# Performance work log

Hardware: AMD Instinct MI355X
Metric: run time of the kernel (lower is better)

## Reference

```python
import math
import jax, jax.numpy as jnp
import numpy as np

NUM_HEADS = 8
FACTOR = 5


def setup_inputs() -> dict:
    key = jax.random.key(0)
    ks = jax.random.split(key, 5)
    B, S, D = 8, 2048, 512
    s = 1.0 / math.sqrt(D)
    return {
        "x": jax.random.normal(ks[0], (B, S, D), dtype=jnp.float32),
        "wq": jax.random.normal(ks[1], (D, D), dtype=jnp.float32) * s,
        "bq": jnp.zeros((D,), jnp.float32),
        "wk": jax.random.normal(ks[2], (D, D), dtype=jnp.float32) * s,
        "bk": jnp.zeros((D,), jnp.float32),
        "wv": jax.random.normal(ks[3], (D, D), dtype=jnp.float32) * s,
        "bv": jnp.zeros((D,), jnp.float32),
        "wo": jax.random.normal(ks[4], (D, D), dtype=jnp.float32) * s,
        "bo": jnp.zeros((D,), jnp.float32),
    }


def reference(x, wq, bq, wk, bk, wv, bv, wo, bo):
    B, S, Dm = x.shape
    H = NUM_HEADS
    Dh = Dm // H
    scale = jnp.sqrt(jnp.float32(Dh))
    # u = min(factor * ceil(ln(S)), S); S is static so compute in Python
    u = min(FACTOR * int(math.ceil(math.log(S))), S)

    def split_heads(t):  # [B,S,Dm] -> [B,H,S,Dh]
        return t.reshape(B, S, H, Dh).transpose(0, 2, 1, 3)

    q = split_heads(x @ wq + bq)
    k = split_heads(x @ wk + bk)
    v = split_heads(x @ wv + bv)

    # S >= 64 -> sparse branch (static decision).
    # Full logits only to compute sparsity measure M (max - mean over keys).
    logits = jnp.einsum("bhqd,bhkd->bhqk", q, k) / scale  # [B,H,S,S]
    M = jnp.max(logits, axis=-1) - jnp.mean(logits, axis=-1)  # [B,H,S]
    _, top_idx = jax.lax.top_k(M, u)  # [B,H,u]

    # Gather top-u queries and run dense attention only for them.
    q_top = jnp.take_along_axis(q, top_idx[..., None], axis=2)  # [B,H,u,Dh]
    top_logits = jnp.einsum("bhqd,bhkd->bhqk", q_top, k) / scale  # [B,H,u,S]
    top_w = jax.nn.softmax(top_logits, axis=-1)
    top_out = jnp.einsum("bhqk,bhkd->bhqd", top_w, v)  # [B,H,u,Dh]

    # Non-selected queries get the mean of V; scatter top outputs in.
    out = jnp.broadcast_to(jnp.mean(v, axis=2, keepdims=True), v.shape)
    b_idx = jnp.arange(B)[:, None, None]
    h_idx = jnp.arange(H)[None, :, None]
    out = out.at[b_idx, h_idx, top_idx].set(top_out)  # [B,H,S,Dh]

    out = out.transpose(0, 2, 1, 3).reshape(B, S, Dm)
    return out @ wo + bo
```

## Files before the change

### kernel.cpp

```cpp
#include <hip/hip_runtime.h>
#include <hip/hip_bf16.h>
#include <math.h>

#define NB 8
#define NS 2048
#define ND 512
#define NH 8
#define DHD 64
#define NU 40
#define NBH 64
#define NM 16384

typedef __attribute__((ext_vector_type(8))) short short8;
typedef __attribute__((ext_vector_type(4))) short short4v;
typedef __attribute__((ext_vector_type(4))) float f32x4;

__device__ __forceinline__ short f2bf(float f) {
  __hip_bfloat16 h = __float2bfloat16(f);
  return *reinterpret_cast<short*>(&h);
}
__device__ __forceinline__ float bf2f(short s) {
  __hip_bfloat16 h;
  *reinterpret_cast<short*>(&h) = s;
  return __bfloat162float(h);
}

__device__ __forceinline__ void gload_lds16(const short* g, short* l) {
  __builtin_amdgcn_global_load_lds(
      (const __attribute__((address_space(1))) unsigned int*)g,
      (__attribute__((address_space(3))) unsigned int*)l, 16, 0, 0);
}

__global__ void prep(const float* __restrict__ x, const float* __restrict__ w0,
                     const float* __restrict__ w1, const float* __restrict__ w2,
                     short* __restrict__ Xs, short* __restrict__ Wts) {
  if (blockIdx.x < 8192) {
    int i = blockIdx.x * 256 + threadIdx.x;
    const float4 v = *(const float4*)(x + (size_t)i * 4);
    int row = i >> 7;
    int col = (i & 127) << 2;
    float vv[4] = {v.x, v.y, v.z, v.w};
    short4v hi, lo;
#pragma unroll
    for (int j = 0; j < 4; ++j) {
      short h = f2bf(vv[j]);
      hi[j] = h;
      lo[j] = f2bf(vv[j] - bf2f(h));
    }
    *(short4v*)(Xs + (size_t)row * 1024 + col) = hi;
    *(short4v*)(Xs + (size_t)row * 1024 + 512 + col) = lo;
  } else {
    int bw = blockIdx.x - 8192;
    int y = bw >> 8;
    int bxy = bw & 255;
    const float* W = y == 0 ? w0 : y == 1 ? w1 : w2;
    short* dst = Wts + (size_t)y * 512 * 1024;
    __shared__ float tile[32][33];
    int bx = bxy & 15, by = bxy >> 4;
    int k0 = bx * 32, n0 = by * 32;
    int r = threadIdx.x >> 3, cg = (threadIdx.x & 7) * 4;
    const float4 v = *(const float4*)(W + (size_t)(k0 + r) * 512 + n0 + cg);
    tile[r][cg] = v.x; tile[r][cg + 1] = v.y; tile[r][cg + 2] = v.z; tile[r][cg + 3] = v.w;
    __syncthreads();
#pragma unroll
    for (int j = 0; j < 4; ++j) {
      int kk = cg + j;
      float f = tile[kk][r];
      short h = f2bf(f);
      dst[(size_t)(n0 + r) * 1024 + k0 + kk] = h;
      dst[(size_t)(n0 + r) * 1024 + 512 + k0 + kk] = f2bf(f - bf2f(h));
    }
  }
}

__global__ __launch_bounds__(256, 2) void qkvgemm(
    const short* __restrict__ A, const short* __restrict__ Wts,
    const float* __restrict__ bq, const float* __restrict__ bk,
    const float* __restrict__ bv, short* __restrict__ Qs,
    short* __restrict__ Ks, short* __restrict__ Vs) {
  __shared__ short As[2][128][64];
  __shared__ short Bs[2][128][64];
  const int bid = blockIdx.x;
  const int wgid = (bid & 7) * 192 + (bid >> 3);
  const int mb = wgid / 12, y = wgid % 12;
  const int m0 = mb * 128;
  const int wsel = y >> 2;
  const int n0 = (y & 3) * 128;
  const short* Wb = Wts + (size_t)wsel * 512 * 1024;
  const float* bias = wsel == 0 ? bq : wsel == 1 ? bk : bv;
  short* dstbase = wsel == 0 ? Qs : wsel == 1 ? Ks : Vs;

  const int tid = threadIdx.x;
  const int w = tid >> 6, lane = tid & 63;
  const int wm = (w >> 1) * 64, wn = (w & 1) * 64;
  const int fr = lane & 15, fk = lane >> 4;

  f32x4 acc[4][4];
  const f32x4 zz = {0.f, 0.f, 0.f, 0.f};
#pragma unroll
  for (int i = 0; i < 4; ++i)
#pragma unroll
    for (int j = 0; j < 4; ++j) acc[i][j] = zz;

  auto stage = [&](int buf, int kt) {
#pragma unroll
    for (int p = 0; p < 4; ++p) {
      int idx = (p * 4 + w) * 64 + lane;
      int r = idx >> 3, c = idx & 7;
      int cs = c ^ (r & 7);
      int sc = (cs < 4) ? (kt + cs * 8) : (512 + kt + (cs - 4) * 8);
      short* lA = &As[buf][0][0] + (p * 4 + w) * 512;
      short* lB = &Bs[buf][0][0] + (p * 4 + w) * 512;
      gload_lds16(A + (size_t)(m0 + r) * 1024 + sc, lA);
      gload_lds16(Wb + (size_t)(n0 + r) * 1024 + sc, lB);
    }
  };

  stage(0, 0);
  __syncthreads();
  for (int kt = 0; kt < 512; kt += 32) {
    int cur = (kt >> 5) & 1;
    if (kt + 32 < 512) stage(cur ^ 1, kt + 32);
    short8 ah[4], al[4], bh[4], bl[4];
#pragma unroll
    for (int mf = 0; mf < 4; ++mf) {
      int r = wm + mf * 16 + fr;
      ah[mf] = *(const short8*)&As[cur][r][(fk ^ (r & 7)) << 3];
      al[mf] = *(const short8*)&As[cur][r][((4 + fk) ^ (r & 7)) << 3];
    }
#pragma unroll
    for (int nf = 0; nf < 4; ++nf) {
      int r = wn + nf * 16 + fr;
      bh[nf] = *(const short8*)&Bs[cur][r][(fk ^ (r & 7)) << 3];
      bl[nf] = *(const short8*)&Bs[cur][r][((4 + fk) ^ (r & 7)) << 3];
    }
#pragma unroll
    for (int mf = 0; mf < 4; ++mf)
#pragma unroll
      for (int nf = 0; nf < 4; ++nf) {
        acc[mf][nf] = __builtin_amdgcn_mfma_f32_16x16x32_bf16(bh[nf], ah[mf], acc[mf][nf], 0, 0, 0);
        acc[mf][nf] = __builtin_amdgcn_mfma_f32_16x16x32_bf16(bh[nf], al[mf], acc[mf][nf], 0, 0, 0);
        acc[mf][nf] = __builtin_amdgcn_mfma_f32_16x16x32_bf16(bl[nf], ah[mf], acc[mf][nf], 0, 0, 0);
      }
    __syncthreads();
  }

#pragma unroll
  for (int mf = 0; mf < 4; ++mf) {
    int m = m0 + wm + mf * 16 + fr;
    int b = m >> 11, s = m & 2047;
#pragma unroll
    for (int nf = 0; nf < 4; ++nf) {
      int nb = n0 + wn + nf * 16 + fk * 4;
      float4 bi4 = *(const float4*)(bias + nb);
      int h = nb >> 6, dh = nb & 63;
      short* dst = dstbase + ((size_t)((b << 3) + h) * 2048 + s) * 128;
      short4v hi, lo;
      float bb[4] = {bi4.x, bi4.y, bi4.z, bi4.w};
#pragma unroll
      for (int j = 0; j < 4; ++j) {
        float v = acc[mf][nf][j] + bb[j];
        short hs = f2bf(v);
        hi[j] = hs;
        lo[j] = f2bf(v - bf2f(hs));
      }
      *(short4v*)(dst + dh) = hi;
      *(short4v*)(dst + 64 + dh) = lo;
    }
  }
}

__global__ __launch_bounds__(256) void colmeans(const short* __restrict__ K,
                                                const short* __restrict__ V,
                                                float* __restrict__ kbarf,
                                                float* __restrict__ vbarf) {
  const int bh = blockIdx.x >> 2, part = blockIdx.x & 3;
  const int c = threadIdx.x & 15;
  const int g = threadIdx.x >> 4;
  const int s0 = part * 512 + g * 32;
  const short* Kb = K + (size_t)bh * 2048 * 128;
  const short* Vb = V + (size_t)bh * 2048 * 128;
  float sk[8], sv[8];
#pragma unroll
  for (int e = 0; e < 8; ++e) { sk[e] = 0.f; sv[e] = 0.f; }
  for (int s = s0; s < s0 + 32; ++s) {
    short8 k8 = *(const short8*)(Kb + (size_t)s * 128 + c * 8);
    short8 v8 = *(const short8*)(Vb + (size_t)s * 128 + c * 8);
#pragma unroll
    for (int e = 0; e < 8; ++e) { sk[e] += bf2f(k8[e]); sv[e] += bf2f(v8[e]); }
  }
  __shared__ float rk[16][128], rv[16][128];
#pragma unroll
  for (int e = 0; e < 8; ++e) { rk[g][c * 8 + e] = sk[e]; rv[g][c * 8 + e] = sv[e]; }
  __syncthreads();
  if (threadIdx.x < 64) {
    int d = threadIdx.x;
    float a = 0.f, b2 = 0.f;
    for (int g2 = 0; g2 < 16; ++g2) {
      a += rk[g2][d] + rk[g2][64 + d];
      b2 += rv[g2][d] + rv[g2][64 + d];
    }
    atomicAdd(kbarf + bh * 64 + d, a * (1.f / 2048.f));
    atomicAdd(vbarf + bh * 64 + d, b2 * (1.f / 2048.f));
  }
}

__global__ __launch_bounds__(256, 2) void qkmax(const short* __restrict__ Qs,
                                                const short* __restrict__ Ks,
                                                const float* __restrict__ kbarf,
                                                float* __restrict__ Mval) {
  __shared__ short Kt[2][128][128];
  __shared__ float red[4][128];
  const int bid = blockIdx.x;
  const int wgid = (bid & 7) * 128 + (bid >> 3);
  const int bh = wgid >> 4, q0 = (wgid & 15) * 128;
  const short* Qb = Qs + ((size_t)bh * 2048 + q0) * 128;
  const short* Kb = Ks + (size_t)bh * 2048 * 128;
  const int tid = threadIdx.x, w = tid >> 6, lane = tid & 63;
  const int fr = lane & 15, fk = lane >> 4;

  short8 qf[8][2][2];
#pragma unroll
  for (int mf = 0; mf < 8; ++mf) {
    int row = mf * 16 + fr;
#pragma unroll
    for (int hl = 0; hl < 2; ++hl)
#pragma unroll
      for (int k0 = 0; k0 < 2; ++k0)
        qf[mf][hl][k0] =
            *(const short8*)(Qb + (size_t)row * 128 + hl * 64 + k0 * 32 + fk * 8);
  }

  f32x4 rmax[8];
#pragma unroll
  for (int mf = 0; mf < 8; ++mf)
#pragma unroll
    for (int j = 0; j < 4; ++j) rmax[mf][j] = -1e30f;
  const f32x4 zz = {0.f, 0.f, 0.f, 0.f};

  auto stageK = [&](int buf, int t) {
#pragma unroll
    for (int p = 0; p < 8; ++p) {
      int idx = p * 256 + tid;
      int r = idx >> 4, c = idx & 15;
      int cs = c ^ (r & 15);
      short* lb = &Kt[buf][0][0] + (size_t)(p * 256 + w * 64) * 8;
      gload_lds16(Kb + (size_t)(t * 128 + r) * 128 + cs * 8, lb);
    }
  };

  stageK(0, 0);
  __syncthreads();
  for (int t = 0; t < 16; ++t) {
    const int cur = t & 1;
    if (t < 15) stageK(cur ^ 1, t + 1);
#pragma unroll
    for (int nf = 0; nf < 2; ++nf) {
      int r = w * 32 + nf * 16 + fr;
      short8 kfh[2], kfl[2];
#pragma unroll
      for (int k0 = 0; k0 < 2; ++k0) {
        kfh[k0] = *(const short8*)&Kt[cur][r][((k0 * 4 + fk) ^ (r & 15)) << 3];
        kfl[k0] = *(const short8*)&Kt[cur][r][((8 + k0 * 4 + fk) ^ (r & 15)) << 3];
      }
#pragma unroll
      for (int mf = 0; mf < 8; ++mf) {
        f32x4 a = zz;
#pragma unroll
        for (int k0 = 0; k0 < 2; ++k0) {
          a = __builtin_amdgcn_mfma_f32_16x16x32_bf16(qf[mf][0][k0], kfh[k0], a, 0, 0, 0);
          a = __builtin_amdgcn_mfma_f32_16x16x32_bf16(qf[mf][0][k0], kfl[k0], a, 0, 0, 0);
          a = __builtin_amdgcn_mfma_f32_16x16x32_bf16(qf[mf][1][k0], kfh[k0], a, 0, 0, 0);
        }
#pragma unroll
        for (int j = 0; j < 4; ++j) rmax[mf][j] = fmaxf(rmax[mf][j], a[j]);
      }
    }
    __syncthreads();
  }

#pragma unroll
  for (int mf = 0; mf < 8; ++mf)
#pragma unroll
    for (int j = 0; j < 4; ++j) {
      float r = rmax[mf][j];
      r = fmaxf(r, __shfl_xor(r, 1, 64));
      r = fmaxf(r, __shfl_xor(r, 2, 64));
      r = fmaxf(r, __shfl_xor(r, 4, 64));
      r = fmaxf(r, __shfl_xor(r, 8, 64));
      if (fr == 0) red[w][mf * 16 + fk * 4 + j] = r;
    }
  __syncthreads();

  if (tid < 128) {
    float mx = fmaxf(fmaxf(red[0][tid], red[1][tid]),
                     fmaxf(red[2][tid], red[3][tid]));
    const short* qp = Qb + (size_t)tid * 128;
    const float* kb = kbarf + bh * 64;
    float dot = 0.f;
#pragma unroll
    for (int ch = 0; ch < 8; ++ch) {
      short8 hi = *(const short8*)(qp + ch * 8);
      short8 lo = *(const short8*)(qp + 64 + ch * 8);
#pragma unroll
      for (int e = 0; e < 8; ++e) dot += (bf2f(hi[e]) + bf2f(lo[e])) * kb[ch * 8 + e];
    }
    Mval[(size_t)bh * 2048 + q0 + tid] = (mx - dot) * 0.125f;
  }
}

__global__ __launch_bounds__(256) void topk40(const float* __restrict__ Mval,
                                              int* __restrict__ tidx,
                                              int* __restrict__ slot8) {
  __shared__ float vals[4][32][64];
  const int w = threadIdx.x >> 6, lane = threadIdx.x & 63;
  const int bh = blockIdx.x * 4 + w;
  const float* src = Mval + (size_t)bh * 2048;
#pragma unroll
  for (int j = 0; j < 32; ++j) vals[w][j][lane] = src[j * 64 + lane];

  for (int it = 0; it < NU; ++it) {
    float best = -INFINITY;
    int bi = 1 << 30;
#pragma unroll
    for (int j = 0; j < 32; ++j) {
      float x = vals[w][j][lane];
      int idx = j * 64 + lane;
      if (x > best) { best = x; bi = idx; }
    }
#pragma unroll
    for (int off = 1; off < 64; off <<= 1) {
      float ov = __shfl_xor(best, off, 64);
      int oi = __shfl_xor(bi, off, 64);
      if (ov > best || (ov == best && oi < bi)) { best = ov; bi = oi; }
    }
    if (lane == 0) {
      tidx[bh * NU + it] = bi;
      slot8[((size_t)(bh >> 3) * 2048 + bi) * 8 + (bh & 7)] = it;
    }
    if ((bi & 63) == lane) vals[w][bi >> 6][lane] = -INFINITY;
  }
}

__global__ __launch_bounds__(256) void topattn1(const short* __restrict__ Qs,
                                                const short* __restrict__ Ks,
                                                const short* __restrict__ Vs,
                                                const int* __restrict__ topidx,
                                                float* __restrict__ pacc,
                                                float* __restrict__ pm,
                                                float* __restrict__ pl) {
  __shared__ float qs[40][68];
  __shared__ float Kst[64][132];
  __shared__ float Vsh[128][68];
  __shared__ float st[40][132];
  __shared__ float m_s[40], l_s[40], r_s[40];
  __shared__ int tix[40];
  const int tid = threadIdx.x;
  const int bh = blockIdx.x, kc = blockIdx.y;
  const short* Kb = Ks + (size_t)bh * 2048 * 128;
  const short* Vb = Vs + (size_t)bh * 2048 * 128;

  if (tid < 40) {
    tix[tid] = topidx[bh * NU + tid];
    m_s[tid] = -INFINITY;
    l_s[tid] = 0.f;
  }
  __syncthreads();
  for (int i = tid; i < 40 * 64; i += 256) {
    int q = i >> 6, dd2 = i & 63;
    const short* qp = Qs + ((size_t)bh * 2048 + tix[q]) * 128;
    qs[q][dd2] = bf2f(qp[dd2]) + bf2f(qp[64 + dd2]);
  }
  const int tx = tid & 31, ty = tid >> 5;
  const int d = tid & 63, qb = tid >> 6;
  float acc[10];
#pragma unroll
  for (int j = 0; j < 10; ++j) acc[j] = 0.f;
  __syncthreads();

  for (int t = 0; t < 4; ++t) {
    int krow0 = kc * 512 + t * 128;
#pragma unroll
    for (int p = 0; p < 4; ++p) {
      int idx = tid + (p << 8);
      int r = idx >> 3, cg = (idx & 7) << 3;
      const short8 kh = *(const short8*)(Kb + (size_t)(krow0 + r) * 128 + cg);
      const short8 kl = *(const short8*)(Kb + (size_t)(krow0 + r) * 128 + 64 + cg);
      const short8 vh = *(const short8*)(Vb + (size_t)(krow0 + r) * 128 + cg);
      const short8 vl = *(const short8*)(Vb + (size_t)(krow0 + r) * 128 + 64 + cg);
#pragma unroll
      for (int j = 0; j < 8; ++j) {
        Kst[cg + j][r] = bf2f(kh[j]) + bf2f(kl[j]);
        Vsh[r][cg + j] = bf2f(vh[j]) + bf2f(vl[j]);
      }
    }
    __syncthreads();

    {
      float c5[5][4];
#pragma unroll
      for (int i = 0; i < 5; ++i)
#pragma unroll
        for (int j = 0; j < 4; ++j) c5[i][j] = 0.f;
      for (int dd = 0; dd < 64; ++dd) {
        const float4 b4 = *(const float4*)&Kst[dd][tx << 2];
#pragma unroll
        for (int i = 0; i < 5; ++i) {
          float a = qs[ty * 5 + i][dd];
          c5[i][0] = fmaf(a, b4.x, c5[i][0]);
          c5[i][1] = fmaf(a, b4.y, c5[i][1]);
          c5[i][2] = fmaf(a, b4.z, c5[i][2]);
          c5[i][3] = fmaf(a, b4.w, c5[i][3]);
        }
      }
#pragma unroll
      for (int i = 0; i < 5; ++i) {
        float4 o;
        o.x = c5[i][0] * 0.125f; o.y = c5[i][1] * 0.125f;
        o.z = c5[i][2] * 0.125f; o.w = c5[i][3] * 0.125f;
        *(float4*)&st[ty * 5 + i][tx << 2] = o;
      }
    }
    __syncthreads();

    if (tid < 160) {
      int q = tid >> 2, sub = tid & 3;
      float tm = -INFINITY;
#pragma unroll
      for (int kk = 0; kk < 32; ++kk) tm = fmaxf(tm, st[q][sub * 32 + kk]);
      tm = fmaxf(tm, __shfl_xor(tm, 1, 64));
      tm = fmaxf(tm, __shfl_xor(tm, 2, 64));
      float mold = m_s[q];
      float mnew = fmaxf(mold, tm);
      float sum = 0.f;
#pragma unroll
      for (int kk = 0; kk < 32; ++kk) {
        float ww = __expf(st[q][sub * 32 + kk] - mnew);
        st[q][sub * 32 + kk] = ww;
        sum += ww;
      }
      sum += __shfl_xor(sum, 1, 64);
      sum += __shfl_xor(sum, 2, 64);
      if (sub == 0) {
        float r = __expf(mold - mnew);
        l_s[q] = l_s[q] * r + sum;
        m_s[q] = mnew;
        r_s[q] = r;
      }
    }
    __syncthreads();

#pragma unroll
    for (int j = 0; j < 10; ++j) {
      int q = qb + (j << 2);
      float a = 0.f;
#pragma unroll
      for (int kk = 0; kk < 128; kk += 4) {
        float4 ww = *(const float4*)&st[q][kk];
        a = fmaf(ww.x, Vsh[kk + 0][d], a);
        a = fmaf(ww.y, Vsh[kk + 1][d], a);
        a = fmaf(ww.z, Vsh[kk + 2][d], a);
        a = fmaf(ww.w, Vsh[kk + 3][d], a);
      }
      acc[j] = acc[j] * r_s[q] + a;
    }
    __syncthreads();
  }

  int pcb = bh * 4 + kc;
#pragma unroll
  for (int j = 0; j < 10; ++j) {
    int q = qb + (j << 2);
    pacc[((size_t)pcb * NU + q) * 64 + d] = acc[j];
  }
  if (tid < 40) {
    pm[pcb * NU + tid] = m_s[tid];
    pl[pcb * NU + tid] = l_s[tid];
  }
}

__global__ __launch_bounds__(256) void topcombine(const float* __restrict__ pacc,
                                                  const float* __restrict__ pm,
                                                  const float* __restrict__ pl,
                                                  float* __restrict__ tout,
                                                  const float* __restrict__ vbarf,
                                                  const float* __restrict__ Wo,
                                                  const float* __restrict__ bo,
                                                  float* __restrict__ om) {
  if (blockIdx.x < 64) {
    const int bh = blockIdx.x;
    const int d = threadIdx.x & 63, qb = threadIdx.x >> 6;
#pragma unroll
    for (int j = 0; j < 10; ++j) {
      int q = qb + (j << 2);
      float m0 = pm[(bh * 4 + 0) * NU + q], m1 = pm[(bh * 4 + 1) * NU + q];
      float m2 = pm[(bh * 4 + 2) * NU + q], m3 = pm[(bh * 4 + 3) * NU + q];
      float mx = fmaxf(fmaxf(m0, m1), fmaxf(m2, m3));
      float e0 = __expf(m0 - mx), e1 = __expf(m1 - mx);
      float e2 = __expf(m2 - mx), e3 = __expf(m3 - mx);
      float L = pl[(bh * 4 + 0) * NU + q] * e0 + pl[(bh * 4 + 1) * NU + q] * e1 +
                pl[(bh * 4 + 2) * NU + q] * e2 + pl[(bh * 4 + 3) * NU + q] * e3;
      float o = (pacc[((size_t)(bh * 4 + 0) * NU + q) * 64 + d] * e0 +
                 pacc[((size_t)(bh * 4 + 1) * NU + q) * 64 + d] * e1 +
                 pacc[((size_t)(bh * 4 + 2) * NU + q) * 64 + d] * e2 +
                 pacc[((size_t)(bh * 4 + 3) * NU + q) * 64 + d] * e3) / L;
      tout[((size_t)bh * NU + q) * 64 + d] = o;
    }
  } else {
    __shared__ float mred[4][64];
    int blk2 = blockIdx.x - 64;
    int b = blk2 >> 3, n0 = (blk2 & 7) * 64;
    int n = n0 + (threadIdx.x & 63), kq = threadIdx.x >> 6;
    const float* vb = vbarf + b * 512;
    float acc = 0.f;
#pragma unroll 8
    for (int k = kq * 128; k < kq * 128 + 128; ++k)
      acc = fmaf(vb[k], Wo[(size_t)k * 512 + n], acc);
    mred[kq][threadIdx.x & 63] = acc;
    __syncthreads();
    if (kq == 0)
      om[b * 512 + n] = bo[n] + mred[0][n - n0] + mred[1][n - n0] +
                        mred[2][n - n0] + mred[3][n - n0];
  }
}

__global__ __launch_bounds__(256) void outall(const float* __restrict__ om,
                                              const int* __restrict__ slot8,
                                              const float* __restrict__ tout,
                                              const float* __restrict__ vbarf,
                                              const float* __restrict__ Wo,
                                              float* __restrict__ out) {
  const int r = blockIdx.x;
  const int b = r >> 11;
  const int n = threadIdx.x;
  float o0 = om[b * 512 + n];
  float o1 = om[b * 512 + n + 256];
  __shared__ float dsh[64];
#pragma unroll
  for (int h = 0; h < 8; ++h) {
    int it = slot8[(size_t)r * 8 + h];
    if (it >= 0) {
      int bh = b * 8 + h;
      int g = bh * NU + it;
      __syncthreads();
      if (n < 64) dsh[n] = tout[(size_t)g * 64 + n] - vbarf[bh * 64 + n];
      __syncthreads();
#pragma unroll 8
      for (int dh = 0; dh < 64; ++dh) {
        float d = dsh[dh];
        const float* wrow = Wo + (size_t)(h * 64 + dh) * 512;
        o0 = fmaf(d, wrow[n], o0);
        o1 = fmaf(d, wrow[n + 256], o1);
      }
    }
  }
  out[(size_t)r * 512 + n] = o0;
  out[(size_t)r * 512 + n + 256] = o1;
}

extern "C" void kernel_launch(void* const* d_in, const int* in_sizes, int n_in,
                              void* d_out, int out_size, void* d_ws, size_t ws_size,
                              hipStream_t stream) {
  (void)in_sizes; (void)n_in; (void)out_size; (void)ws_size;
  const float* x  = (const float*)d_in[0];
  const float* wq = (const float*)d_in[1];
  const float* bq = (const float*)d_in[2];
  const float* wk = (const float*)d_in[3];
  const float* bk = (const float*)d_in[4];
  const float* wv = (const float*)d_in[5];
  const float* bv = (const float*)d_in[6];
  const float* wo = (const float*)d_in[7];
  const float* bo = (const float*)d_in[8];
  float* out = (float*)d_out;

  short* Xs   = (short*)d_ws;
  short* Wts  = Xs + (size_t)16384 * 1024;
  short* Qsb  = Wts + (size_t)3 * 512 * 1024;
  short* Ksb  = Qsb + (size_t)NBH * NS * 128;
  short* Vsb  = Ksb + (size_t)NBH * NS * 128;
  float* Mval = (float*)(Vsb + (size_t)NBH * NS * 128);
  float* kbarf = Mval + (size_t)NBH * NS;
  float* vbarf = kbarf + NBH * 64;
  int* tidx   = (int*)(vbarf + NBH * 64);
  int* slot8  = tidx + NBH * NU;
  float* pacc = (float*)(slot8 + (size_t)NM * 8);
  float* pm   = pacc + (size_t)NBH * 4 * NU * 64;
  float* pl   = pm + NBH * 4 * NU;
  float* tout = pl + NBH * 4 * NU;
  float* om   = tout + (size_t)NBH * NU * 64;

  hipMemsetAsync(kbarf, 0, 2 * NBH * 64 * sizeof(float), stream);
  hipMemsetAsync(slot8, 0xFF, (size_t)NM * 8 * sizeof(int), stream);
  prep<<<8960, 256, 0, stream>>>(x, wq, wk, wv, Xs, Wts);
  qkvgemm<<<1536, 256, 0, stream>>>(Xs, Wts, bq, bk, bv, Qsb, Ksb, Vsb);
  colmeans<<<NBH * 4, 256, 0, stream>>>(Ksb, Vsb, kbarf, vbarf);
  qkmax<<<1024, 256, 0, stream>>>(Qsb, Ksb, kbarf, Mval);
  topk40<<<16, 256, 0, stream>>>(Mval, tidx, slot8);
  topattn1<<<dim3(NBH, 4), 256, 0, stream>>>(Qsb, Ksb, Vsb, tidx, pacc, pm, pl);
  topcombine<<<128, 256, 0, stream>>>(pacc, pm, pl, tout, vbarf, wo, bo, om);
  outall<<<NM, 256, 0, stream>>>(om, slot8, tout, vbarf, wo, out);
}
```

Measured before the change: 351.5 us.

## Pipeline GEMM and qkmax loads with vmcnt waits; fuse column means into QKV GEMM

Restructures the qkvgemm and qkmax main loops to prefetch two stages ahead. Each iteration waits on a partial vmcnt count and a raw s_barrier instead of a full __syncthreads, and raises wave priority around the MFMA blocks. The separate colmeans kernel is removed. Per-column sums of K and V are instead accumulated in the qkvgemm epilogue and reduced with shuffles and atomics. This saves one launch and a full re-read of K and V, and gives more room to overlap load latency with compute. The cost is more atomics and hand-tuned wait counts that must match the number of loads issued per stage.

```diff
diff --git a/kernel.cpp b/kernel.cpp
--- a/kernel.cpp
+++ b/kernel.cpp
@@ -77,7 +77,8 @@
     const short* __restrict__ A, const short* __restrict__ Wts,
     const float* __restrict__ bq, const float* __restrict__ bk,
     const float* __restrict__ bv, short* __restrict__ Qs,
-    short* __restrict__ Ks, short* __restrict__ Vs) {
+    short* __restrict__ Ks, short* __restrict__ Vs,
+    float* __restrict__ kbarf, float* __restrict__ vbarf) {
   __shared__ short As[2][128][64];
   __shared__ short Bs[2][128][64];
   const int bid = blockIdx.x;
@@ -102,7 +103,8 @@
 #pragma unroll
     for (int j = 0; j < 4; ++j) acc[i][j] = zz;
 
-  auto stage = [&](int buf, int kt) {
+  auto stage = [&](int buf, int t) {
+    const int kt = t * 32;
 #pragma unroll
     for (int p = 0; p < 4; ++p) {
       int idx = (p * 4 + w) * 64 + lane;
@@ -117,10 +119,16 @@
   };
 
   stage(0, 0);
-  __syncthreads();
-  for (int kt = 0; kt < 512; kt += 32) {
-    int cur = (kt >> 5) & 1;
-    if (kt + 32 < 512) stage(cur ^ 1, kt + 32);
+  stage(1, 1);
+  for (int t = 0; t < 16; ++t) {
+    const int cur = t & 1;
+    if (t < 15) {
+      asm volatile("s_waitcnt vmcnt(8)" ::: "memory");
+    } else {
+      asm volatile("s_waitcnt vmcnt(0)" ::: "memory");
+    }
+    __builtin_amdgcn_s_barrier();
+
     short8 ah[4], al[4], bh[4], bl[4];
 #pragma unroll
     for (int mf = 0; mf < 4; ++mf) {
@@ -134,6 +142,7 @@
       bh[nf] = *(const short8*)&Bs[cur][r][(fk ^ (r & 7)) << 3];
       bl[nf] = *(const short8*)&Bs[cur][r][((4 + fk) ^ (r & 7)) << 3];
     }
+    __builtin_amdgcn_s_setprio(1);
 #pragma unroll
     for (int mf = 0; mf < 4; ++mf)
 #pragma unroll
@@ -142,8 +151,17 @@
         acc[mf][nf] = __builtin_amdgcn_mfma_f32_16x16x32_bf16(bh[nf], al[mf], acc[mf][nf], 0, 0, 0);
         acc[mf][nf] = __builtin_amdgcn_mfma_f32_16x16x32_bf16(bl[nf], ah[mf], acc[mf][nf], 0, 0, 0);
       }
-    __syncthreads();
-  }
+    __builtin_amdgcn_s_setprio(0);
+    __builtin_amdgcn_sched_barrier(0);
+    __builtin_amdgcn_s_barrier();
+    if (t < 14) stage(cur, t + 2);
+  }
+
+  float csum[4][4];
+#pragma unroll
+  for (int nf = 0; nf < 4; ++nf)
+#pragma unroll
+    for (int j = 0; j < 4; ++j) csum[nf][j] = 0.f;
 
 #pragma unroll
   for (int mf = 0; mf < 4; ++mf) {
@@ -160,6 +178,7 @@
 #pragma unroll
       for (int j = 0; j < 4; ++j) {
         float v = acc[mf][nf][j] + bb[j];
+        csum[nf][j] += v;
         short hs = f2bf(v);
         hi[j] = hs;
         lo[j] = f2bf(v - bf2f(hs));
@@ -168,40 +187,25 @@
       *(short4v*)(dst + 64 + dh) = lo;
     }
   }
-}
-
-__global__ __launch_bounds__(256) void colmeans(const short* __restrict__ K,
-                                                const short* __restrict__ V,
-                                                float* __restrict__ kbarf,
-                                                float* __restrict__ vbarf) {
-  const int bh = blockIdx.x >> 2, part = blockIdx.x & 3;
-  const int c = threadIdx.x & 15;
-  const int g = threadIdx.x >> 4;
-  const int s0 = part * 512 + g * 32;
-  const short* Kb = K + (size_t)bh * 2048 * 128;
-  const short* Vb = V + (size_t)bh * 2048 * 128;
-  float sk[8], sv[8];
-#pragma unroll
-  for (int e = 0; e < 8; ++e) { sk[e] = 0.f; sv[e] = 0.f; }
-  for (int s = s0; s < s0 + 32; ++s) {
-    short8 k8 = *(const short8*)(Kb + (size_t)s * 128 + c * 8);
-    short8 v8 = *(const short8*)(Vb + (size_t)s * 128 + c * 8);
-#pragma unroll
-    for (int e = 0; e < 8; ++e) { sk[e] += bf2f(k8[e]); sv[e] += bf2f(v8[e]); }
-  }
-  __shared__ float rk[16][128], rv[16][128];
-#pragma unroll
-  for (int e = 0; e < 8; ++e) { rk[g][c * 8 + e] = sk[e]; rv[g][c * 8 + e] = sv[e]; }
-  __syncthreads();
-  if (threadIdx.x < 64) {
-    int d = threadIdx.x;
-    float a = 0.f, b2 = 0.f;
-    for (int g2 = 0; g2 < 16; ++g2) {
-      a += rk[g2][d] + rk[g2][64 + d];
-      b2 += rv[g2][d] + rv[g2][64 + d];
-    }
-    atomicAdd(kbarf + bh * 64 + d, a * (1.f / 2048.f));
-    atomicAdd(vbarf + bh * 64 + d, b2 * (1.f / 2048.f));
+
+  if (wsel != 0) {
+    float* bar = (wsel == 1) ? kbarf : vbarf;
+    int b = m0 >> 11;
+#pragma unroll
+    for (int nf = 0; nf < 4; ++nf)
+#pragma unroll
+      for (int j = 0; j < 4; ++j) {
+        float s = csum[nf][j];
+        s += __shfl_xor(s, 1, 64);
+        s += __shfl_xor(s, 2, 64);
+        s += __shfl_xor(s, 4, 64);
+        s += __shfl_xor(s, 8, 64);
+        if (fr == 0) {
+          int cfull = n0 + wn + nf * 16 + fk * 4 + j;
+          int h = cfull >> 6, dh = cfull & 63;
+          atomicAdd(bar + ((b << 3) + h) * 64 + dh, s * (1.f / 2048.f));
+        }
+      }
   }
 }
 
@@ -250,10 +254,17 @@
   };
 
   stageK(0, 0);
-  __syncthreads();
+  stageK(1, 1);
   for (int t = 0; t < 16; ++t) {
     const int cur = t & 1;
-    if (t < 15) stageK(cur ^ 1, t + 1);
+    if (t < 15) {
+      asm volatile("s_waitcnt vmcnt(8)" ::: "memory");
+    } else {
+      asm volatile("s_waitcnt vmcnt(0)" ::: "memory");
+    }
+    __builtin_amdgcn_s_barrier();
+
+    __builtin_amdgcn_s_setprio(1);
 #pragma unroll
     for (int nf = 0; nf < 2; ++nf) {
       int r = w * 32 + nf * 16 + fr;
@@ -276,7 +287,10 @@
         for (int j = 0; j < 4; ++j) rmax[mf][j] = fmaxf(rmax[mf][j], a[j]);
       }
     }
-    __syncthreads();
+    __builtin_amdgcn_s_setprio(0);
+    __builtin_amdgcn_sched_barrier(0);
+    __builtin_amdgcn_s_barrier();
+    if (t < 14) stageK(cur, t + 2);
   }
 
 #pragma unroll
@@ -592,8 +606,7 @@
   hipMemsetAsync(kbarf, 0, 2 * NBH * 64 * sizeof(float), stream);
   hipMemsetAsync(slot8, 0xFF, (size_t)NM * 8 * sizeof(int), stream);
   prep<<<8960, 256, 0, stream>>>(x, wq, wk, wv, Xs, Wts);
-  qkvgemm<<<1536, 256, 0, stream>>>(Xs, Wts, bq, bk, bv, Qsb, Ksb, Vsb);
-  colmeans<<<NBH * 4, 256, 0, stream>>>(Ksb, Vsb, kbarf, vbarf);
+  qkvgemm<<<1536, 256, 0, stream>>>(Xs, Wts, bq, bk, bv, Qsb, Ksb, Vsb, kbarf, vbarf);
   qkmax<<<1024, 256, 0, stream>>>(Qsb, Ksb, kbarf, Mval);
   topk40<<<16, 256, 0, stream>>>(Mval, tidx, slot8);
   topattn1<<<dim3(NBH, 4), 256, 0, stream>>>(Qsb, Ksb, Vsb, tidx, pacc, pm, pl);
```

Result: no change. 347.6 us (-1.1%).
